# Optimization experiments

Measured on AMD Instinct MI355X. Metric: run time of the kernel, lower is better.

Reference implementation:

```python
import jax, jax.numpy as jnp
import numpy as np

TAU = 2.0 / 3.0
EPS = float(np.finfo(np.float32).tiny)  # train-mode epsilon


def setup_inputs() -> dict:
    key = jax.random.key(0)
    k1, k2 = jax.random.split(key)
    B, N, K = 64, 16384, 16
    logits = jax.random.normal(k1, (B, N), dtype=jnp.float32)
    u = jax.random.uniform(k2, (B, N), dtype=jnp.float32)
    # Gumbel(0,1) noise, matching torch's -log(-log(rand + 1e-20) + 1e-20)
    gumbel = -jnp.log(-jnp.log(u + 1e-20) + 1e-20)
    return {"logits": logits, "gumbel": gumbel, "k": K}


def reference(logits, gumbel, k):
    # Sequential k-step Gumbel-softmax top-k (train mode).
    log_eps = jnp.log(jnp.asarray(EPS, dtype=logits.dtype))  # log(max(1-hard, eps)) at selected idx
    noisy = logits + gumbel  # [B, N]
    n = logits.shape[1]

    def step(carry, _):
        # carry: masked noisy logits [B, N]
        soft = jax.nn.softmax(carry / TAU, axis=1)           # [B, N]
        idx = jnp.argmax(soft, axis=1)                       # top-1 per row
        hard = jax.nn.one_hot(idx, n, dtype=soft.dtype)      # [B, N]
        # mask = max(1 - hard, eps) -> log(mask) is log_eps at selected pos, 0 elsewhere
        next_carry = carry + hard * log_eps
        return next_carry, soft

    _, softs = jax.lax.scan(step, noisy, None, length=k)     # softs: [K, B, N]

    idx = jnp.argmax(softs, axis=2)                          # [K, B]
    hards = jax.nn.one_hot(idx, n, dtype=softs.dtype)        # [K, B, N]
    # straight-through: hard forward, soft gradient
    st = jax.lax.stop_gradient(hards - softs) + softs
    return st, softs
```

## Files before the change

### kernel.cpp

```cpp
#include <hip/hip_runtime.h>
#include <math.h>

#define B 64
#define N 16384
#define K 16
#define CHUNK 256
#define NCH   (N / CHUNK)
#define WV_OFF 0
#define WI_OFF 65536
#define WS_OFF 131072
#define WM_OFF 135168
#define WC_OFF 139264

typedef float f4 __attribute__((ext_vector_type(4)));

__device__ __forceinline__ unsigned ordu(float x) {
  unsigned i = __float_as_uint(x);
  return (i & 0x80000000u) ? ~i : (i | 0x80000000u);
}
__device__ __forceinline__ int mbcnt64(unsigned long long m) {
  return __builtin_amdgcn_mbcnt_hi((unsigned)(m >> 32),
         __builtin_amdgcn_mbcnt_lo((unsigned)m, 0u));
}

__global__ __launch_bounds__(256)
void gtk_partial(const float* __restrict__ logits, const float* __restrict__ gumbel,
                 float* __restrict__ ws, float* __restrict__ st) {
  const int tid  = threadIdx.x;
  const int wave = tid >> 6, lane = tid & 63;
  const int gch  = blockIdx.x * 4 + wave;
  const int c    = gch & (NCH - 1);
  const size_t base = (size_t)gch * CHUNK;

  float x[4]; unsigned u[4];
#pragma unroll
  for (int e = 0; e < 4; ++e) {
    const int o = e * 64 + lane;
    x[e] = logits[base + o] + gumbel[base + o];
    u[e] = ordu(x[e]);
  }

  {
    float* zst = st + ((size_t)blockIdx.x << 14);
    const f4 z = {0.f, 0.f, 0.f, 0.f};
#pragma unroll
    for (int i = 0; i < 16; ++i)
      *(f4*)(zst + i * 1024 + (tid << 2)) = z;
  }

  float mc = fmaxf(fmaxf(x[0], x[1]), fmaxf(x[2], x[3]));
#pragma unroll
  for (int off = 32; off; off >>= 1) mc = fmaxf(mc, __shfl_xor(mc, off));

  float s = 0.f;
#pragma unroll
  for (int e = 0; e < 4; ++e) s += __expf((x[e] - mc) * 1.5f);
#pragma unroll
  for (int off = 32; off; off >>= 1) s += __shfl_xor(s, off);

  unsigned p = 0;
#pragma unroll
  for (int bit = 31; bit >= 0; --bit) {
    const unsigned test = p | (1u << bit);
    int cnt = 0;
#pragma unroll
    for (int e = 0; e < 4; ++e) cnt += __popcll(__ballot(u[e] >= test));
    if (cnt >= K) p = test;
  }

  unsigned long long bgt[4], beq[4];
#pragma unroll
  for (int e = 0; e < 4; ++e) { bgt[e] = __ballot(u[e] > p); beq[e] = __ballot(u[e] == p); }
  const int tg = __popcll(bgt[0]) + __popcll(bgt[1]) + __popcll(bgt[2]) + __popcll(bgt[3]);
  const int need = K - tg;
  float* wV = ws + WV_OFF + (size_t)gch * K;
  int*   wI = (int*)(ws + WI_OFF) + (size_t)gch * K;
  int gpre = 0, epre = 0;
#pragma unroll
  for (int e = 0; e < 4; ++e) {
    const int myi = (c << 8) + e * 64 + lane;
    if (u[e] > p) {
      const int r = gpre + mbcnt64(bgt[e]);
      wV[r] = x[e]; wI[r] = myi;
    } else if (u[e] == p) {
      const int r = epre + mbcnt64(beq[e]);
      if (r < need) { wV[tg + r] = x[e]; wI[tg + r] = myi; }
    }
    gpre += __popcll(bgt[e]); epre += __popcll(beq[e]);
  }

  if (lane == 0) {
    (ws + WS_OFF)[gch] = s;
    (ws + WM_OFF)[gch] = mc;
  }
}

__global__ __launch_bounds__(256)
void gtk_merge(float* __restrict__ ws, float* __restrict__ st) {
  const int b = blockIdx.x;
  const int tid = threadIdx.x, wave = tid >> 6, lane = tid & 63;

  __shared__ float lv[64];
  __shared__ int   li[64];
  __shared__ float tv[K];
  __shared__ int   ti[K];
  __shared__ float sv16[K];
  __shared__ int   si16[K];

  const float* wV = ws + WV_OFF + (size_t)b * (NCH * K);
  const int*   wI = (const int*)(ws + WI_OFF) + (size_t)b * (NCH * K);

  float xv[4]; unsigned xu[4]; int xi[4];
#pragma unroll
  for (int e = 0; e < 4; ++e) {
    const int q = wave * 256 + e * 64 + lane;
    xv[e] = wV[q]; xi[e] = wI[q]; xu[e] = ordu(xv[e]);
  }

  unsigned p = 0;
#pragma unroll
  for (int bit = 31; bit >= 0; --bit) {
    const unsigned test = p | (1u << bit);
    int cnt = 0;
#pragma unroll
    for (int e = 0; e < 4; ++e) cnt += __popcll(__ballot(xu[e] >= test));
    if (cnt >= K) p = test;
  }
  unsigned long long bgt[4], beq[4];
#pragma unroll
  for (int e = 0; e < 4; ++e) { bgt[e] = __ballot(xu[e] > p); beq[e] = __ballot(xu[e] == p); }
  const int tg = __popcll(bgt[0]) + __popcll(bgt[1]) + __popcll(bgt[2]) + __popcll(bgt[3]);
  const int need = K - tg;
  int gpre = 0, epre = 0;
#pragma unroll
  for (int e = 0; e < 4; ++e) {
    if (xu[e] > p) {
      const int r = gpre + mbcnt64(bgt[e]);
      lv[wave * K + r] = xv[e]; li[wave * K + r] = xi[e];
    } else if (xu[e] == p) {
      const int r = epre + mbcnt64(beq[e]);
      if (r < need) { lv[wave * K + tg + r] = xv[e]; li[wave * K + tg + r] = xi[e]; }
    }
    gpre += __popcll(bgt[e]); epre += __popcll(beq[e]);
  }
  __syncthreads();

  if (wave == 0) {
    const float v = lv[lane]; const int i = li[lane];
    const unsigned uu = ordu(v);
    unsigned p2 = 0;
#pragma unroll
    for (int bit = 31; bit >= 0; --bit) {
      const unsigned test = p2 | (1u << bit);
      if (__popcll(__ballot(uu >= test)) >= K) p2 = test;
    }
    const unsigned long long g = __ballot(uu > p2);
    const unsigned long long q = __ballot(uu == p2);
    const int tg2 = __popcll(g), nd2 = K - tg2;
    if (uu > p2) {
      const int r = mbcnt64(g);
      tv[r] = v; ti[r] = i;
    } else if (uu == p2) {
      const int r = mbcnt64(q);
      if (r < nd2) { tv[tg2 + r] = v; ti[tg2 + r] = i; }
    }
    if (lane < K) {
      const float mv = tv[lane]; const int mi = ti[lane];
      int rk = 0;
#pragma unroll
      for (int j = 0; j < K; ++j) {
        const float ov = tv[j]; const int oi = ti[j];
        rk += (ov > mv || (ov == mv && oi < mi)) ? 1 : 0;
      }
      sv16[rk] = mv; si16[rk] = mi;
    }
    const float m0 = sv16[0];

    const float S   = (ws + WS_OFF)[b * NCH + lane];
    const float mcc = (ws + WM_OFF)[b * NCH + lane];
    float a = S * __expf((mcc - m0) * 1.5f);
#pragma unroll
    for (int off = 32; off; off >>= 1) a += __shfl_xor(a, off);

    if (lane == 0) {
      float* wrow = ws + WC_OFF + (size_t)b * 48;
      float D = a;
#pragma unroll
      for (int j = 0; j < K; ++j) {
        wrow[j] = 1.0f / D;
        D -= __expf((sv16[j] - m0) * 1.5f);
      }
      int* wi = (int*)(wrow + K);
#pragma unroll
      for (int j = 0; j < K; ++j) wi[j] = si16[j];
      wrow[32] = m0;
    }

    if (lane < K) {
      st[(size_t)lane * (size_t)(B * N) + (size_t)b * N + si16[lane]] = 1.0f;
    }
  }
}

__global__ __launch_bounds__(256)
void gtk_soft(const float* __restrict__ logits, const float* __restrict__ gumbel,
              const float* __restrict__ ws, float* __restrict__ softs) {
  const int bid = blockIdx.x, tid = threadIdx.x;
  const int xcd = bid & 7;
  const int j   = bid >> 3;
  const int k   = j & 15;
  const int s8  = j >> 4;
  const int seg = s8 * 8 + xcd;
  const int b   = seg >> 1;
  const int n0  = (seg & 1) << 13;
  const size_t base = (size_t)b * N + n0;

  __shared__ float sck, sm0;
  __shared__ int   sidx[K];
  const float* wrow = ws + WC_OFF + (size_t)b * 48;
  if (tid < K) sidx[tid] = ((const int*)(wrow + K))[tid];
  if (tid == 0) { sck = wrow[k]; sm0 = wrow[32]; }
  __syncthreads();
  const float ck = sck, m0 = sm0;

  const float* lg = logits + base;
  const float* gm = gumbel + base;
  float* dst = softs + (size_t)k * (size_t)(B * N) + base;

#pragma unroll
  for (int i = 0; i < 8; ++i) {
    const int off = i * 1024 + (tid << 2);
    const f4 lv = *(const f4*)(lg + off);
    const f4 gv = *(const f4*)(gm + off);
    f4 s;
#pragma unroll
    for (int e = 0; e < 4; ++e)
      s[e] = __expf((lv[e] + gv[e] - m0) * 1.5f) * ck;
    *(f4*)(dst + off) = s;
  }

#pragma unroll
  for (int jj = 0; jj < K; ++jj) {
    const int d = sidx[jj] - n0;
    if ((jj < k) && ((unsigned)d < 8192u) && (((d >> 2) & 255) == tid))
      dst[d] = 0.f;
  }
}

extern "C" void kernel_launch(void* const* d_in, const int* in_sizes, int n_in,
                              void* d_out, int out_size, void* d_ws, size_t ws_size,
                              hipStream_t stream) {
  const float* logits = (const float*)d_in[0];
  const float* gumbel = (const float*)d_in[1];
  float* st    = (float*)d_out;
  float* softs = st + (size_t)K * B * N;
  float* ws    = (float*)d_ws;

  gtk_partial<<<(B * NCH) / 4, 256, 0, stream>>>(logits, gumbel, ws, st);
  gtk_merge<<<B, 256, 0, stream>>>(ws, st);
  gtk_soft<<<2048, 256, 0, stream>>>(logits, gumbel, ws, softs);
}
```

Before: 43.25 us.

## Cache per-chunk exp values as bf16 and rescale in soft kernel

The partial kernel now stores each element's exp((x-chunk_max)*1.5) as bf16 into workspace. The soft kernel reads these 2-byte values instead of the fp32 logits and gumbel, rescaling them with a per-chunk factor exp((mc-m0)*1.5)*c_k. This cuts the soft kernel's input traffic from 8 bytes to 2 bytes per element across the 16 outputs per row and removes the per-output exp. In exchange the softs output loses precision to bf16, which may exceed tolerance, and the partial kernel gains an extra write.

```diff
diff --git a/kernel.cpp b/kernel.cpp
--- a/kernel.cpp
+++ b/kernel.cpp
@@ -11,8 +11,10 @@
 #define WS_OFF 131072
 #define WM_OFF 135168
 #define WC_OFF 139264
+#define WE_OFF 143360
 
 typedef float f4 __attribute__((ext_vector_type(4)));
+typedef unsigned short u16x8 __attribute__((ext_vector_type(8)));
 
 __device__ __forceinline__ unsigned ordu(float x) {
   unsigned i = __float_as_uint(x);
@@ -21,6 +23,14 @@
 __device__ __forceinline__ int mbcnt64(unsigned long long m) {
   return __builtin_amdgcn_mbcnt_hi((unsigned)(m >> 32),
          __builtin_amdgcn_mbcnt_lo((unsigned)m, 0u));
+}
+__device__ __forceinline__ unsigned short f2bf(float f) {
+  unsigned b = __float_as_uint(f);
+  b += 0x7FFFu + ((b >> 16) & 1u);
+  return (unsigned short)(b >> 16);
+}
+__device__ __forceinline__ float bf2f(unsigned short v) {
+  return __uint_as_float(((unsigned)v) << 16);
 }
 
 __global__ __launch_bounds__(256)
@@ -52,9 +62,14 @@
 #pragma unroll
   for (int off = 32; off; off >>= 1) mc = fmaxf(mc, __shfl_xor(mc, off));
 
+  unsigned short* wE = (unsigned short*)(ws + WE_OFF);
   float s = 0.f;
 #pragma unroll
-  for (int e = 0; e < 4; ++e) s += __expf((x[e] - mc) * 1.5f);
+  for (int e = 0; e < 4; ++e) {
+    const float Ee = __expf((x[e] - mc) * 1.5f);
+    s += Ee;
+    wE[base + e * 64 + lane] = f2bf(Ee);
+  }
 #pragma unroll
   for (int off = 32; off; off >>= 1) s += __shfl_xor(s, off);
 
@@ -203,8 +218,7 @@
 }
 
 __global__ __launch_bounds__(256)
-void gtk_soft(const float* __restrict__ logits, const float* __restrict__ gumbel,
-              const float* __restrict__ ws, float* __restrict__ softs) {
+void gtk_soft(const float* __restrict__ ws, float* __restrict__ softs) {
   const int bid = blockIdx.x, tid = threadIdx.x;
   const int xcd = bid & 7;
   const int j   = bid >> 3;
@@ -215,34 +229,40 @@
   const int n0  = (seg & 1) << 13;
   const size_t base = (size_t)b * N + n0;
 
-  __shared__ float sck, sm0;
+  __shared__ float ssc[32];
   __shared__ int   sidx[K];
   const float* wrow = ws + WC_OFF + (size_t)b * 48;
   if (tid < K) sidx[tid] = ((const int*)(wrow + K))[tid];
-  if (tid == 0) { sck = wrow[k]; sm0 = wrow[32]; }
+  if (tid < 32) {
+    const float m0  = wrow[32];
+    const float ck  = wrow[k];
+    const float mcc = (ws + WM_OFF)[b * NCH + (n0 >> 8) + tid];
+    ssc[tid] = __expf((mcc - m0) * 1.5f) * ck;
+  }
   __syncthreads();
-  const float ck = sck, m0 = sm0;
-
-  const float* lg = logits + base;
-  const float* gm = gumbel + base;
+
+  const unsigned short* Eb = (const unsigned short*)(ws + WE_OFF) + base;
   float* dst = softs + (size_t)k * (size_t)(B * N) + base;
 
 #pragma unroll
-  for (int i = 0; i < 8; ++i) {
-    const int off = i * 1024 + (tid << 2);
-    const f4 lv = *(const f4*)(lg + off);
-    const f4 gv = *(const f4*)(gm + off);
-    f4 s;
-#pragma unroll
-    for (int e = 0; e < 4; ++e)
-      s[e] = __expf((lv[e] + gv[e] - m0) * 1.5f) * ck;
-    *(f4*)(dst + off) = s;
+  for (int i = 0; i < 4; ++i) {
+    const int off = i * 2048 + (tid << 3);
+    const u16x8 ev = *(const u16x8*)(Eb + off);
+    const float sc = ssc[i * 8 + (tid >> 5)];
+    f4 s0, s1;
+#pragma unroll
+    for (int e = 0; e < 4; ++e) {
+      s0[e] = bf2f(ev[e])     * sc;
+      s1[e] = bf2f(ev[4 + e]) * sc;
+    }
+    *(f4*)(dst + off)     = s0;
+    *(f4*)(dst + off + 4) = s1;
   }
 
 #pragma unroll
   for (int jj = 0; jj < K; ++jj) {
     const int d = sidx[jj] - n0;
-    if ((jj < k) && ((unsigned)d < 8192u) && (((d >> 2) & 255) == tid))
+    if ((jj < k) && ((unsigned)d < 8192u) && (((d & 2047) >> 3) == tid))
       dst[d] = 0.f;
   }
 }
@@ -258,5 +278,5 @@
 
   gtk_partial<<<(B * NCH) / 4, 256, 0, stream>>>(logits, gumbel, ws, st);
   gtk_merge<<<B, 256, 0, stream>>>(ws, st);
-  gtk_soft<<<2048, 256, 0, stream>>>(logits, gumbel, ws, softs);
-}
+  gtk_soft<<<2048, 256, 0, stream>>>(ws, softs);
+}
```

New measurement: 41.64 us. 3.7% less time.
